# Kernel tuning notes

Measured on AMD Instinct MI355X. Metric: run time of the kernel, lower is better.

## Reference

```python
import jax, jax.numpy as jnp
import numpy as np

H = 32  # hidden size (hard-coded in the torch module)

def _lstm_layer(x, W_ih, W_hh):
    # x: [B, T, F]; W_ih: [4H, F]; W_hh: [4H, H]; bias=False
    B = x.shape[0]
    # precompute input projection for all timesteps: [T, B, 4H]
    xg = jnp.einsum('btf,gf->tbg', x, W_ih)
    WhhT = W_hh.T  # [H, 4H]
    def step(carry, xg_t):
        h, c = carry
        gates = xg_t + h @ WhhT          # [B, 4H]
        i, f, g, o = jnp.split(gates, 4, axis=-1)  # PyTorch gate order i,f,g,o
        i = jax.nn.sigmoid(i)
        f = jax.nn.sigmoid(f)
        g = jnp.tanh(g)
        o = jax.nn.sigmoid(o)
        c = f * c + i * g
        h = o * jnp.tanh(c)
        return (h, c), h
    h0 = jnp.zeros((B, H), x.dtype)
    c0 = jnp.zeros((B, H), x.dtype)
    (hT, cT), hs = jax.lax.scan(step, (h0, c0), xg)
    return jnp.transpose(hs, (1, 0, 2)), hT, cT  # outputs [B,T,H], final h, final c


def setup_inputs() -> dict:
    key = jax.random.key(0)
    ks = jax.random.split(key, 8)
    B, T, F = 8192, 60, 158
    s_in = 1.0 / np.sqrt(H)  # PyTorch LSTM init scale
    inp = {
        'x':     jax.random.normal(ks[0], (B, T, F), jnp.float32),
        'W_ih0': jax.random.uniform(ks[1], (4 * H, F), jnp.float32, -s_in, s_in),
        'W_hh0': jax.random.uniform(ks[2], (4 * H, H), jnp.float32, -s_in, s_in),
        'W_ih1': jax.random.uniform(ks[3], (4 * H, H), jnp.float32, -s_in, s_in),
        'W_hh1': jax.random.uniform(ks[4], (4 * H, H), jnp.float32, -s_in, s_in),
        'W1':    jax.random.uniform(ks[5], (16, H), jnp.float32, -s_in, s_in),
        'b1':    jax.random.uniform(ks[6], (16,), jnp.float32, -s_in, s_in),
        'W2':    jax.random.uniform(ks[7], (1, 16), jnp.float32, -0.25, 0.25),
    }
    return inp


def reference(x, W_ih0, W_hh0, W_ih1, W_hh1, W1, b1, W2):
    out1, h1, c1 = _lstm_layer(x, W_ih0, W_hh0)      # layer 1 (inter-layer dropout inactive at eval)
    out2, h2, c2 = _lstm_layer(out1, W_ih1, W_hh1)   # layer 2
    # torch code: output, h_n = lstm(x) -> h_n is the TUPLE (h_n, c_n),
    # so h_n[-1] == c_n with shape [num_layers=2, B, H]
    c_n = jnp.stack([c1, c2], axis=0)                 # [2, B, H]
    y = jax.nn.relu(c_n @ W1.T + b1) @ W2.T           # [2, B, 1]
    return y
```

## Files before the change

### kernel.cpp

```cpp
#include <hip/hip_runtime.h>


constexpr int Bn = 8192, Tn = 60, Fn = 158, Hn = 32;
constexpr int SKX = 168;
constexpr int SKH = 40;
constexpr float LS = 4096.f;
constexpr float ILS = 1.f / 4096.f;

typedef _Float16 half8 __attribute__((ext_vector_type(8)));
typedef __fp16 half2f __attribute__((ext_vector_type(2)));
typedef float floatx4 __attribute__((ext_vector_type(4)));

__device__ __forceinline__ float sigm_(float x) {
    return __fdividef(1.f, 1.f + __expf(-x));
}
__device__ __forceinline__ float tanh_(float x) {
    return 1.f - __fdividef(2.f, __expf(2.f * x) + 1.f);
}
__device__ __forceinline__ unsigned h2u(half2f h) {
    return __builtin_bit_cast(unsigned, h);
}
__device__ __forceinline__ void cvt8h(const float* v, half8& hi, half8& lo) {
#pragma unroll
    for (int j = 0; j < 8; j += 2) {
        half2f h = __builtin_amdgcn_cvt_pkrtz(v[j], v[j + 1]);
        float r0 = (v[j] - (float)h[0]) * LS;
        float r1 = (v[j + 1] - (float)h[1]) * LS;
        half2f l = __builtin_amdgcn_cvt_pkrtz(r0, r1);
        hi[j] = (_Float16)h[0]; hi[j + 1] = (_Float16)h[1];
        lo[j] = (_Float16)l[0]; lo[j + 1] = (_Float16)l[1];
    }
}

__global__ __launch_bounds__(256, 2) void lstm2_fused_kernel(
    const float* __restrict__ x,
    const float* __restrict__ Wih0, const float* __restrict__ Whh0,
    const float* __restrict__ Wih1, const float* __restrict__ Whh1,
    const float* __restrict__ W1, const float* __restrict__ b1,
    const float* __restrict__ W2, float* __restrict__ out) {
    __shared__ unsigned short sXh[2 * 16 * SKX];
    __shared__ unsigned short sXl[2 * 16 * SKX];
    __shared__ unsigned short sH[2][2][2][16 * SKH];

    const int tid = threadIdx.x;
    const int wave = tid >> 6, lane = tid & 63;
    const int quad = lane >> 4, l15 = lane & 15;
    const int bBase = blockIdx.x * 16;
    const int hl = l15 >> 2, gi = l15 & 3;

    half8 bX[5][2][2];
#pragma unroll
    for (int mt = 0; mt < 2; ++mt) {
        const int grow = gi * 32 + wave * 8 + mt * 4 + hl;
#pragma unroll
        for (int ks = 0; ks < 5; ++ks) {
            float wv[8];
#pragma unroll
            for (int j = 0; j < 8; ++j) {
                int k = ks * 32 + quad * 8 + j;
                wv[j] = (k < Fn) ? Wih0[grow * Fn + k] : 0.f;
            }
            cvt8h(wv, bX[ks][mt][0], bX[ks][mt][1]);
        }
    }
    half8 bW[3][2][2];
    const float* Wp[3] = {Whh0, Wih1, Whh1};
#pragma unroll
    for (int m = 0; m < 3; ++m)
#pragma unroll
        for (int mt = 0; mt < 2; ++mt) {
            const int grow = gi * 32 + wave * 8 + mt * 4 + hl;
            const float* wp = Wp[m] + grow * Hn + quad * 8;
            float4 q0 = *(const float4*)(wp);
            float4 q1 = *(const float4*)(wp + 4);
            float wv[8] = {q0.x, q0.y, q0.z, q0.w, q1.x, q1.y, q1.z, q1.w};
            cvt8h(wv, bW[m][mt][0], bW[m][mt][1]);
        }

    const float* xp[5];
    int soff[5];
    bool act[5];
#pragma unroll
    for (int r = 0; r < 5; ++r) {
        int i = tid + r * 256;
        act[r] = (i < 1264);
        int row = i / 79, c = i - row * 79;
        if (!act[r]) { row = 0; c = 0; }
        soff[r] = row * (SKX / 2) + c;
        xp[r] = x + (size_t)(bBase + row) * (Tn * Fn) + 2 * c;
    }
    auto stage = [&](const float2* v, int buf) {
        unsigned* dh = (unsigned*)sXh + buf * (16 * SKX / 2);
        unsigned* dl = (unsigned*)sXl + buf * (16 * SKX / 2);
#pragma unroll
        for (int r = 0; r < 5; ++r) {
            if (act[r]) {
                half2f h = __builtin_amdgcn_cvt_pkrtz(v[r].x, v[r].y);
                half2f l = __builtin_amdgcn_cvt_pkrtz(
                    (v[r].x - (float)h[0]) * LS, (v[r].y - (float)h[1]) * LS);
                dh[soff[r]] = h2u(h);
                dl[soff[r]] = h2u(l);
            }
        }
    };

    for (int i = tid; i < 2560; i += 256) ((unsigned*)sH)[i] = 0;
    if (tid < 32) {
        int buf = tid >> 4, row = tid & 15;
        ((unsigned*)sXh)[buf * 1344 + row * 84 + 79] = 0;
        ((unsigned*)sXl)[buf * 1344 + row * 84 + 79] = 0;
    }

#pragma unroll
    for (int t0 = 0; t0 < 2; ++t0) {
        float2 v[5];
#pragma unroll
        for (int r = 0; r < 5; ++r) {
            v[r] = act[r] ? *(const float2*)xp[r] : make_float2(0.f, 0.f);
            xp[r] += Fn;
        }
        stage(v, t0);
    }

    const int hOffR = l15 * SKH + quad * 8;
    const int hW = l15 * SKH + wave * 8 + quad;
    float c1[2] = {0.f, 0.f}, c2[2] = {0.f, 0.f};

    auto packStore = [&](float h0, float h1v, unsigned short* dh, unsigned short* dl) {
        half2f hh = __builtin_amdgcn_cvt_pkrtz(h0, h1v);
        half2f ll = __builtin_amdgcn_cvt_pkrtz((h0 - (float)hh[0]) * LS,
                                               (h1v - (float)hh[1]) * LS);
        unsigned uh = h2u(hh), ul = h2u(ll);
        dh[hW] = (unsigned short)uh; dh[hW + 4] = (unsigned short)(uh >> 16);
        dl[hW] = (unsigned short)ul; dl[hW + 4] = (unsigned short)(ul >> 16);
    };

    __syncthreads();

    {
        floatx4 aH[2] = {}, aL[2] = {};
#pragma unroll
        for (int ks = 0; ks < 5; ++ks) {
            const int off = l15 * SKX + ks * 32 + quad * 8;
            half8 xh = *(const half8*)(sXh + off);
            half8 xl = *(const half8*)(sXl + off);
#pragma unroll
            for (int mt = 0; mt < 2; ++mt) {
                aH[mt] = __builtin_amdgcn_mfma_f32_16x16x32_f16(bX[ks][mt][0], xh, aH[mt], 0, 0, 0);
                aL[mt] = __builtin_amdgcn_mfma_f32_16x16x32_f16(bX[ks][mt][1], xh, aL[mt], 0, 0, 0);
                aL[mt] = __builtin_amdgcn_mfma_f32_16x16x32_f16(bX[ks][mt][0], xl, aL[mt], 0, 0, 0);
            }
        }
        float hv[2];
#pragma unroll
        for (int mt = 0; mt < 2; ++mt) {
            float gI = fmaf(ILS, aL[mt][0], aH[mt][0]);
            float gF = fmaf(ILS, aL[mt][1], aH[mt][1]);
            float gG = fmaf(ILS, aL[mt][2], aH[mt][2]);
            float gO = fmaf(ILS, aL[mt][3], aH[mt][3]);
            c1[mt] = sigm_(gF) * c1[mt] + sigm_(gI) * tanh_(gG);
            hv[mt] = sigm_(gO) * tanh_(c1[mt]);
        }
        packStore(hv[0], hv[1], sH[0][0][0], sH[0][0][1]);
    }
    __syncthreads();

    for (int i = 0; i < Tn - 1; ++i) {
        float2 xr[5];
        const bool pf = (i + 2 < Tn);
        if (pf) {
#pragma unroll
            for (int r = 0; r < 5; ++r) {
                xr[r] = act[r] ? *(const float2*)xp[r] : make_float2(0.f, 0.f);
                xp[r] += Fn;
            }
        }
        const int par = i & 1;
        const unsigned short* bxh = sXh + ((i + 1) & 1) * (16 * SKX);
        const unsigned short* bxl = sXl + ((i + 1) & 1) * (16 * SKX);
        half8 f1h = *(const half8*)(sH[par][0][0] + hOffR);
        half8 f1l = *(const half8*)(sH[par][0][1] + hOffR);
        half8 f2h = *(const half8*)(sH[par][1][0] + hOffR);
        half8 f2l = *(const half8*)(sH[par][1][1] + hOffR);
        floatx4 a1H[2] = {}, a1L[2] = {}, a2H[2] = {}, a2L[2] = {};
#pragma unroll
        for (int ks = 0; ks < 5; ++ks) {
            const int off = l15 * SKX + ks * 32 + quad * 8;
            half8 xh = *(const half8*)(bxh + off);
            half8 xl = *(const half8*)(bxl + off);
#pragma unroll
            for (int mt = 0; mt < 2; ++mt) {
                a1H[mt] = __builtin_amdgcn_mfma_f32_16x16x32_f16(bX[ks][mt][0], xh, a1H[mt], 0, 0, 0);
                a1L[mt] = __builtin_amdgcn_mfma_f32_16x16x32_f16(bX[ks][mt][1], xh, a1L[mt], 0, 0, 0);
                a1L[mt] = __builtin_amdgcn_mfma_f32_16x16x32_f16(bX[ks][mt][0], xl, a1L[mt], 0, 0, 0);
            }
        }
#pragma unroll
        for (int mt = 0; mt < 2; ++mt) {
            a1H[mt] = __builtin_amdgcn_mfma_f32_16x16x32_f16(bW[0][mt][0], f1h, a1H[mt], 0, 0, 0);
            a1L[mt] = __builtin_amdgcn_mfma_f32_16x16x32_f16(bW[0][mt][1], f1h, a1L[mt], 0, 0, 0);
            a1L[mt] = __builtin_amdgcn_mfma_f32_16x16x32_f16(bW[0][mt][0], f1l, a1L[mt], 0, 0, 0);
            a2H[mt] = __builtin_amdgcn_mfma_f32_16x16x32_f16(bW[1][mt][0], f1h, a2H[mt], 0, 0, 0);
            a2L[mt] = __builtin_amdgcn_mfma_f32_16x16x32_f16(bW[1][mt][1], f1h, a2L[mt], 0, 0, 0);
            a2L[mt] = __builtin_amdgcn_mfma_f32_16x16x32_f16(bW[1][mt][0], f1l, a2L[mt], 0, 0, 0);
            a2H[mt] = __builtin_amdgcn_mfma_f32_16x16x32_f16(bW[2][mt][0], f2h, a2H[mt], 0, 0, 0);
            a2L[mt] = __builtin_amdgcn_mfma_f32_16x16x32_f16(bW[2][mt][1], f2h, a2L[mt], 0, 0, 0);
            a2L[mt] = __builtin_amdgcn_mfma_f32_16x16x32_f16(bW[2][mt][0], f2l, a2L[mt], 0, 0, 0);
        }
        float h1v[2], h2v[2];
#pragma unroll
        for (int mt = 0; mt < 2; ++mt) {
            float gI = fmaf(ILS, a2L[mt][0], a2H[mt][0]);
            float gF = fmaf(ILS, a2L[mt][1], a2H[mt][1]);
            float gG = fmaf(ILS, a2L[mt][2], a2H[mt][2]);
            float gO = fmaf(ILS, a2L[mt][3], a2H[mt][3]);
            c2[mt] = sigm_(gF) * c2[mt] + sigm_(gI) * tanh_(gG);
            h2v[mt] = sigm_(gO) * tanh_(c2[mt]);
            gI = fmaf(ILS, a1L[mt][0], a1H[mt][0]);
            gF = fmaf(ILS, a1L[mt][1], a1H[mt][1]);
            gG = fmaf(ILS, a1L[mt][2], a1H[mt][2]);
            gO = fmaf(ILS, a1L[mt][3], a1H[mt][3]);
            c1[mt] = sigm_(gF) * c1[mt] + sigm_(gI) * tanh_(gG);
            h1v[mt] = sigm_(gO) * tanh_(c1[mt]);
        }
        packStore(h1v[0], h1v[1], sH[par ^ 1][0][0], sH[par ^ 1][0][1]);
        packStore(h2v[0], h2v[1], sH[par ^ 1][1][0], sH[par ^ 1][1][1]);
        if (pf) stage(xr, i & 1);
        __syncthreads();
    }

    {
        const int par = (Tn - 1) & 1;
        half8 f1h = *(const half8*)(sH[par][0][0] + hOffR);
        half8 f1l = *(const half8*)(sH[par][0][1] + hOffR);
        half8 f2h = *(const half8*)(sH[par][1][0] + hOffR);
        half8 f2l = *(const half8*)(sH[par][1][1] + hOffR);
        floatx4 aH[2] = {}, aL[2] = {};
#pragma unroll
        for (int mt = 0; mt < 2; ++mt) {
            aH[mt] = __builtin_amdgcn_mfma_f32_16x16x32_f16(bW[1][mt][0], f1h, aH[mt], 0, 0, 0);
            aL[mt] = __builtin_amdgcn_mfma_f32_16x16x32_f16(bW[1][mt][1], f1h, aL[mt], 0, 0, 0);
            aL[mt] = __builtin_amdgcn_mfma_f32_16x16x32_f16(bW[1][mt][0], f1l, aL[mt], 0, 0, 0);
            aH[mt] = __builtin_amdgcn_mfma_f32_16x16x32_f16(bW[2][mt][0], f2h, aH[mt], 0, 0, 0);
            aL[mt] = __builtin_amdgcn_mfma_f32_16x16x32_f16(bW[2][mt][1], f2h, aL[mt], 0, 0, 0);
            aL[mt] = __builtin_amdgcn_mfma_f32_16x16x32_f16(bW[2][mt][0], f2l, aL[mt], 0, 0, 0);
        }
#pragma unroll
        for (int mt = 0; mt < 2; ++mt) {
            float gI = fmaf(ILS, aL[mt][0], aH[mt][0]);
            float gF = fmaf(ILS, aL[mt][1], aH[mt][1]);
            float gG = fmaf(ILS, aL[mt][2], aH[mt][2]);
            c2[mt] = sigm_(gF) * c2[mt] + sigm_(gI) * tanh_(gG);
        }
    }

    float* sC = (float*)sXh;
#pragma unroll
    for (int mt = 0; mt < 2; ++mt) {
        sC[l15 * 33 + wave * 8 + mt * 4 + quad] = c1[mt];
        sC[528 + l15 * 33 + wave * 8 + mt * 4 + quad] = c2[mt];
    }
    __syncthreads();
    if (tid < 32) {
        int l = tid >> 4, b = tid & 15;
        const float* cc = sC + l * 528 + b * 33;
        float y = 0.f;
#pragma unroll 1
        for (int q = 0; q < 16; ++q) {
            float s = b1[q];
#pragma unroll
            for (int j = 0; j < 32; ++j) s = fmaf(cc[j], W1[q * 32 + j], s);
            y = fmaf(fmaxf(s, 0.f), W2[q], y);
        }
        out[l * Bn + bBase + b] = y;
    }
}

extern "C" void kernel_launch(void* const* d_in, const int* in_sizes, int n_in,
                              void* d_out, int out_size, void* d_ws, size_t ws_size,
                              hipStream_t stream) {
    const float* x    = (const float*)d_in[0];
    const float* Wih0 = (const float*)d_in[1];
    const float* Whh0 = (const float*)d_in[2];
    const float* Wih1 = (const float*)d_in[3];
    const float* Whh1 = (const float*)d_in[4];
    const float* W1   = (const float*)d_in[5];
    const float* b1   = (const float*)d_in[6];
    const float* W2   = (const float*)d_in[7];
    float* out = (float*)d_out;

    lstm2_fused_kernel<<<Bn / 16, 256, 0, stream>>>(x, Wih0, Whh0, Wih1, Whh1,
                                                    W1, b1, W2, out);
}
```

Measured before the change: 461.8 us.

## Split MFMA accumulator chains and move x-projection before the step barrier

The low-part correction MFMAs now accumulate into a separate third accumulator instead of chaining on the same one. This shortens the dependent MFMA chains so more independent MFMAs can be in flight. The input projection for each step is now computed and the next x tile staged before the barrier, and the barrier moves from the end of the loop body to the middle. The aim is to overlap x-projection work with waiting on the hidden state from the previous step, at the cost of extra accumulator registers and a reordered synchronisation that must still protect the double-buffered x and h buffers.

```diff
diff --git a/kernel.cpp b/kernel.cpp
--- a/kernel.cpp
+++ b/kernel.cpp
@@ -138,7 +138,7 @@
     __syncthreads();
 
     {
-        floatx4 aH[2] = {}, aL[2] = {};
+        floatx4 aH[2] = {}, aL[2] = {}, aX[2] = {};
 #pragma unroll
         for (int ks = 0; ks < 5; ++ks) {
             const int off = l15 * SKX + ks * 32 + quad * 8;
@@ -148,16 +148,17 @@
             for (int mt = 0; mt < 2; ++mt) {
                 aH[mt] = __builtin_amdgcn_mfma_f32_16x16x32_f16(bX[ks][mt][0], xh, aH[mt], 0, 0, 0);
                 aL[mt] = __builtin_amdgcn_mfma_f32_16x16x32_f16(bX[ks][mt][1], xh, aL[mt], 0, 0, 0);
-                aL[mt] = __builtin_amdgcn_mfma_f32_16x16x32_f16(bX[ks][mt][0], xl, aL[mt], 0, 0, 0);
+                aX[mt] = __builtin_amdgcn_mfma_f32_16x16x32_f16(bX[ks][mt][0], xl, aX[mt], 0, 0, 0);
             }
         }
         float hv[2];
 #pragma unroll
         for (int mt = 0; mt < 2; ++mt) {
-            float gI = fmaf(ILS, aL[mt][0], aH[mt][0]);
-            float gF = fmaf(ILS, aL[mt][1], aH[mt][1]);
-            float gG = fmaf(ILS, aL[mt][2], aH[mt][2]);
-            float gO = fmaf(ILS, aL[mt][3], aH[mt][3]);
+            floatx4 lo = aL[mt] + aX[mt];
+            float gI = fmaf(ILS, lo[0], aH[mt][0]);
+            float gF = fmaf(ILS, lo[1], aH[mt][1]);
+            float gG = fmaf(ILS, lo[2], aH[mt][2]);
+            float gO = fmaf(ILS, lo[3], aH[mt][3]);
             c1[mt] = sigm_(gF) * c1[mt] + sigm_(gI) * tanh_(gG);
             hv[mt] = sigm_(gO) * tanh_(c1[mt]);
         }
@@ -178,56 +179,61 @@
         const int par = i & 1;
         const unsigned short* bxh = sXh + ((i + 1) & 1) * (16 * SKX);
         const unsigned short* bxl = sXl + ((i + 1) & 1) * (16 * SKX);
+        floatx4 a1H[2] = {}, a1L[2] = {}, a1X[2] = {};
+#pragma unroll
+        for (int ks = 0; ks < 5; ++ks) {
+            const int off = l15 * SKX + ks * 32 + quad * 8;
+            half8 xh = *(const half8*)(bxh + off);
+            half8 xl = *(const half8*)(bxl + off);
+#pragma unroll
+            for (int mt = 0; mt < 2; ++mt) {
+                a1H[mt] = __builtin_amdgcn_mfma_f32_16x16x32_f16(bX[ks][mt][0], xh, a1H[mt], 0, 0, 0);
+                a1L[mt] = __builtin_amdgcn_mfma_f32_16x16x32_f16(bX[ks][mt][1], xh, a1L[mt], 0, 0, 0);
+                a1X[mt] = __builtin_amdgcn_mfma_f32_16x16x32_f16(bX[ks][mt][0], xl, a1X[mt], 0, 0, 0);
+            }
+        }
+        if (pf) stage(xr, i & 1);
+        __syncthreads();
+
         half8 f1h = *(const half8*)(sH[par][0][0] + hOffR);
         half8 f1l = *(const half8*)(sH[par][0][1] + hOffR);
         half8 f2h = *(const half8*)(sH[par][1][0] + hOffR);
         half8 f2l = *(const half8*)(sH[par][1][1] + hOffR);
-        floatx4 a1H[2] = {}, a1L[2] = {}, a2H[2] = {}, a2L[2] = {};
-#pragma unroll
-        for (int ks = 0; ks < 5; ++ks) {
-            const int off = l15 * SKX + ks * 32 + quad * 8;
-            half8 xh = *(const half8*)(bxh + off);
-            half8 xl = *(const half8*)(bxl + off);
-#pragma unroll
-            for (int mt = 0; mt < 2; ++mt) {
-                a1H[mt] = __builtin_amdgcn_mfma_f32_16x16x32_f16(bX[ks][mt][0], xh, a1H[mt], 0, 0, 0);
-                a1L[mt] = __builtin_amdgcn_mfma_f32_16x16x32_f16(bX[ks][mt][1], xh, a1L[mt], 0, 0, 0);
-                a1L[mt] = __builtin_amdgcn_mfma_f32_16x16x32_f16(bX[ks][mt][0], xl, a1L[mt], 0, 0, 0);
-            }
-        }
+        floatx4 a2H[2] = {}, a2L[2] = {}, a2X[2] = {};
 #pragma unroll
         for (int mt = 0; mt < 2; ++mt) {
             a1H[mt] = __builtin_amdgcn_mfma_f32_16x16x32_f16(bW[0][mt][0], f1h, a1H[mt], 0, 0, 0);
             a1L[mt] = __builtin_amdgcn_mfma_f32_16x16x32_f16(bW[0][mt][1], f1h, a1L[mt], 0, 0, 0);
-            a1L[mt] = __builtin_amdgcn_mfma_f32_16x16x32_f16(bW[0][mt][0], f1l, a1L[mt], 0, 0, 0);
+            a1X[mt] = __builtin_amdgcn_mfma_f32_16x16x32_f16(bW[0][mt][0], f1l, a1X[mt], 0, 0, 0);
             a2H[mt] = __builtin_amdgcn_mfma_f32_16x16x32_f16(bW[1][mt][0], f1h, a2H[mt], 0, 0, 0);
             a2L[mt] = __builtin_amdgcn_mfma_f32_16x16x32_f16(bW[1][mt][1], f1h, a2L[mt], 0, 0, 0);
-            a2L[mt] = __builtin_amdgcn_mfma_f32_16x16x32_f16(bW[1][mt][0], f1l, a2L[mt], 0, 0, 0);
+            a2X[mt] = __builtin_amdgcn_mfma_f32_16x16x32_f16(bW[1][mt][0], f1l, a2X[mt], 0, 0, 0);
             a2H[mt] = __builtin_amdgcn_mfma_f32_16x16x32_f16(bW[2][mt][0], f2h, a2H[mt], 0, 0, 0);
             a2L[mt] = __builtin_amdgcn_mfma_f32_16x16x32_f16(bW[2][mt][1], f2h, a2L[mt], 0, 0, 0);
-            a2L[mt] = __builtin_amdgcn_mfma_f32_16x16x32_f16(bW[2][mt][0], f2l, a2L[mt], 0, 0, 0);
+            a2X[mt] = __builtin_amdgcn_mfma_f32_16x16x32_f16(bW[2][mt][0], f2l, a2X[mt], 0, 0, 0);
         }
         float h1v[2], h2v[2];
 #pragma unroll
         for (int mt = 0; mt < 2; ++mt) {
-            float gI = fmaf(ILS, a2L[mt][0], a2H[mt][0]);
-            float gF = fmaf(ILS, a2L[mt][1], a2H[mt][1]);
-            float gG = fmaf(ILS, a2L[mt][2], a2H[mt][2]);
-            float gO = fmaf(ILS, a2L[mt][3], a2H[mt][3]);
+            floatx4 lo1 = a1L[mt] + a1X[mt];
+            float gI = fmaf(ILS, lo1[0], a1H[mt][0]);
+            float gF = fmaf(ILS, lo1[1], a1H[mt][1]);
+            float gG = fmaf(ILS, lo1[2], a1H[mt][2]);
+            float gO = fmaf(ILS, lo1[3], a1H[mt][3]);
+            c1[mt] = sigm_(gF) * c1[mt] + sigm_(gI) * tanh_(gG);
+            h1v[mt] = sigm_(gO) * tanh_(c1[mt]);
+            floatx4 lo2 = a2L[mt] + a2X[mt];
+            gI = fmaf(ILS, lo2[0], a2H[mt][0]);
+            gF = fmaf(ILS, lo2[1], a2H[mt][1]);
+            gG = fmaf(ILS, lo2[2], a2H[mt][2]);
+            gO = fmaf(ILS, lo2[3], a2H[mt][3]);
             c2[mt] = sigm_(gF) * c2[mt] + sigm_(gI) * tanh_(gG);
             h2v[mt] = sigm_(gO) * tanh_(c2[mt]);
-            gI = fmaf(ILS, a1L[mt][0], a1H[mt][0]);
-            gF = fmaf(ILS, a1L[mt][1], a1H[mt][1]);
-            gG = fmaf(ILS, a1L[mt][2], a1H[mt][2]);
-            gO = fmaf(ILS, a1L[mt][3], a1H[mt][3]);
-            c1[mt] = sigm_(gF) * c1[mt] + sigm_(gI) * tanh_(gG);
-            h1v[mt] = sigm_(gO) * tanh_(c1[mt]);
         }
         packStore(h1v[0], h1v[1], sH[par ^ 1][0][0], sH[par ^ 1][0][1]);
         packStore(h2v[0], h2v[1], sH[par ^ 1][1][0], sH[par ^ 1][1][1]);
-        if (pf) stage(xr, i & 1);
-        __syncthreads();
-    }
+    }
+    __syncthreads();
 
     {
         const int par = (Tn - 1) & 1;
@@ -235,21 +241,22 @@
         half8 f1l = *(const half8*)(sH[par][0][1] + hOffR);
         half8 f2h = *(const half8*)(sH[par][1][0] + hOffR);
         half8 f2l = *(const half8*)(sH[par][1][1] + hOffR);
-        floatx4 aH[2] = {}, aL[2] = {};
+        floatx4 aH[2] = {}, aL[2] = {}, aX[2] = {};
 #pragma unroll
         for (int mt = 0; mt < 2; ++mt) {
             aH[mt] = __builtin_amdgcn_mfma_f32_16x16x32_f16(bW[1][mt][0], f1h, aH[mt], 0, 0, 0);
             aL[mt] = __builtin_amdgcn_mfma_f32_16x16x32_f16(bW[1][mt][1], f1h, aL[mt], 0, 0, 0);
-            aL[mt] = __builtin_amdgcn_mfma_f32_16x16x32_f16(bW[1][mt][0], f1l, aL[mt], 0, 0, 0);
+            aX[mt] = __builtin_amdgcn_mfma_f32_16x16x32_f16(bW[1][mt][0], f1l, aX[mt], 0, 0, 0);
             aH[mt] = __builtin_amdgcn_mfma_f32_16x16x32_f16(bW[2][mt][0], f2h, aH[mt], 0, 0, 0);
             aL[mt] = __builtin_amdgcn_mfma_f32_16x16x32_f16(bW[2][mt][1], f2h, aL[mt], 0, 0, 0);
-            aL[mt] = __builtin_amdgcn_mfma_f32_16x16x32_f16(bW[2][mt][0], f2l, aL[mt], 0, 0, 0);
-        }
-#pragma unroll
-        for (int mt = 0; mt < 2; ++mt) {
-            float gI = fmaf(ILS, aL[mt][0], aH[mt][0]);
-            float gF = fmaf(ILS, aL[mt][1], aH[mt][1]);
-            float gG = fmaf(ILS, aL[mt][2], aH[mt][2]);
+            aX[mt] = __builtin_amdgcn_mfma_f32_16x16x32_f16(bW[2][mt][0], f2l, aX[mt], 0, 0, 0);
+        }
+#pragma unroll
+        for (int mt = 0; mt < 2; ++mt) {
+            floatx4 lo = aL[mt] + aX[mt];
+            float gI = fmaf(ILS, lo[0], aH[mt][0]);
+            float gF = fmaf(ILS, lo[1], aH[mt][1]);
+            float gG = fmaf(ILS, lo[2], aH[mt][2]);
             c2[mt] = sigm_(gF) * c2[mt] + sigm_(gI) * tanh_(gG);
         }
     }
```

Measured after the change: 489.7 us. +6.0%, slower.
